# Optimization experiments

Measured on AMD Instinct MI355X. Metric: run time of the kernel, lower is better.

## Reference

```python
import jax, jax.numpy as jnp
import numpy as np

DIM = 1024
HEADS = 16
DH = DIM // HEADS
SEQ = 1024
MEM_LEN = 1024
CMEM_LEN = 256
RATIO = 4
SCALE = DH ** -0.5
LN_EPS = 1e-5


def shift(x):
    # x: [b,h,i,j] -> relative-position shift trick
    b, h, i, j = x.shape
    x = jnp.concatenate([x, jnp.zeros((b, h, i, i), x.dtype)], axis=-1)
    l = i + j - 1
    x = x.reshape(b, h, -1)
    pad = (-x.shape[-1]) % l
    x = jnp.concatenate([x, jnp.zeros((b, h, pad), x.dtype)], axis=-1)
    x = x.reshape(b, h, -1, l)
    return x[:, :, :i, i - 1:]


def layer_norm(x, g, b):
    mu = jnp.mean(x, axis=-1, keepdims=True)
    var = jnp.var(x, axis=-1, keepdims=True)
    return (x - mu) * jax.lax.rsqrt(var + LN_EPS) * g + b


def setup_inputs() -> dict:
    key = jax.random.key(0)
    ks = jax.random.split(key, 12)
    B = 4
    KV = CMEM_LEN + MEM_LEN + SEQ
    std = 0.02
    return {
        'x': jax.random.normal(ks[0], (B, SEQ, DIM), jnp.float32),
        'mem': jax.random.normal(ks[1], (B, MEM_LEN, DIM), jnp.float32),
        'cmem': jax.random.normal(ks[2], (B, CMEM_LEN, DIM), jnp.float32),
        'pos_embed': jax.random.normal(ks[3], (HEADS, KV, DH), jnp.float32),
        'input_mask': jnp.ones((B, SEQ), jnp.bool_),
        'Wq': jax.random.normal(ks[4], (DIM, DIM), jnp.float32) * std,
        'Wkv': jax.random.normal(ks[5], (DIM, 2 * DIM), jnp.float32) * std,
        'Wout': jax.random.normal(ks[6], (DIM, DIM), jnp.float32) * std,
        'bout': jnp.zeros((DIM,), jnp.float32),
        'ln_g': jnp.ones((DIM,), jnp.float32),
        'ln_b': jnp.zeros((DIM,), jnp.float32),
        'conv_w': jax.random.normal(ks[7], (DIM, DIM, RATIO), jnp.float32) * std,
        'conv_b': jnp.zeros((DIM,), jnp.float32),
    }


def reference(x, mem, cmem, pos_embed, input_mask, Wq, Wkv, Wout, bout, ln_g, ln_b, conv_w, conv_b):
    b, t, e = x.shape
    mem_len, cmem_len = mem.shape[1], cmem.shape[1]
    total_mem = mem_len + cmem_len

    q = x @ Wq  # [b,t,e]
    kv_input = jnp.concatenate([cmem, mem, x], axis=1)  # [b,kv,e]
    kv_len = kv_input.shape[1]
    kv = kv_input @ Wkv
    k, v = jnp.split(kv, 2, axis=-1)

    def merge_heads(u):
        return u.reshape(u.shape[0], u.shape[1], HEADS, DH).transpose(0, 2, 1, 3)

    q, k, v = merge_heads(q), merge_heads(k), merge_heads(v)  # [b,h,*,dh]

    dots = jnp.einsum('bhid,bhjd->bhij', q, k) * SCALE  # [b,h,t,kv]
    mask_value = -jnp.finfo(dots.dtype).max

    pe = pos_embed[:, -kv_len:].astype(q.dtype)
    pos_dots = jnp.einsum('bhid,hjd->bhij', q, pe) * SCALE
    dots = dots + shift(pos_dots)

    # input mask (memory columns always visible)
    imask = input_mask[:, None, :, None] & input_mask[:, None, None, :]  # [b,1,t,t]
    imask = jnp.concatenate([jnp.ones((b, 1, t, total_mem), jnp.bool_), imask], axis=-1)
    dots = jnp.where(imask, dots, mask_value)

    # causal mask with memory offset
    causal = jnp.triu(jnp.ones((t, t + total_mem), jnp.bool_), k=1 + total_mem)
    dots = jnp.where(causal[None, None], mask_value, dots)

    attn = jax.nn.softmax(dots, axis=-1)
    out = jnp.einsum('bhij,bhjd->bhid', attn, v)
    out = out.transpose(0, 2, 1, 3).reshape(b, t, -1)
    logits = out @ Wout + bout
    logits = layer_norm(x + logits, ln_g, ln_b)

    # memory update (calc_memory=True, eval mode: no aux reconstruction loss)
    all_mem = jnp.concatenate([mem, x], axis=1)
    old_mem, new_mem = all_mem[:, :-MEM_LEN], all_mem[:, -MEM_LEN:]
    # old_mem length (mem_len+t-MEM_LEN) is a multiple of RATIO here -> no pad needed
    om = old_mem.transpose(0, 2, 1)  # [b,e,L]
    comp = jax.lax.conv_general_dilated(
        om, conv_w, window_strides=(RATIO,), padding='VALID',
        dimension_numbers=('NCH', 'OIH', 'NCH')) + conv_b[None, :, None]
    compressed_mem = comp.transpose(0, 2, 1)  # [b,L/ratio,e]
    all_cmem = jnp.concatenate([cmem, compressed_mem], axis=1)
    new_cmem = all_cmem[:, -CMEM_LEN:]

    aux_loss = jnp.zeros((1,), q.dtype)
    return logits, new_mem, new_cmem, aux_loss
```

## Files before the change

### kernel.cpp

```cpp
#include <hip/hip_runtime.h>
#include <stdint.h>

typedef __attribute__((ext_vector_type(8))) short short8;
typedef __attribute__((ext_vector_type(4))) short short4_;
typedef __attribute__((ext_vector_type(4))) float floatx4;

#define MFMA16(a,b,c) __builtin_amdgcn_mfma_f32_16x16x32_bf16((a),(b),(c),0,0,0)

__device__ __forceinline__ short f2b(float f) {
  union { float f; uint32_t u; } v; v.f = f;
  uint32_t r = v.u + 0x7fffu + ((v.u >> 16) & 1u);
  return (short)(r >> 16);
}

__device__ __forceinline__ unsigned cvt_pk_bf16(float a, float b) {
  unsigned r;
  asm("v_cvt_pk_bf16_f32 %0, %1, %2" : "=v"(r) : "v"(a), "v"(b));
  return r;
}


__global__ __launch_bounds__(256) void pack_kvin(const float* __restrict__ x,
    const float* __restrict__ mem, const float* __restrict__ cmem,
    short* __restrict__ out) {
  long idx = (long)blockIdx.x * 256 + threadIdx.x;
  long base = idx * 4;
  if (base >= 9437184L) return;
  int b = (int)(base / 2359296L);
  int rem = (int)(base - (long)b * 2359296L);
  int r = rem >> 10, c = rem & 1023;
  const float* src;
  if (r < 256)       src = cmem + ((long)b * 256  + r)          * 1024 + c;
  else if (r < 1280) src = mem  + ((long)b * 1024 + (r - 256))  * 1024 + c;
  else               src = x    + ((long)b * 1024 + (r - 1280)) * 1024 + c;
  float4 v = *(const float4*)src;
  short4_ o; o.x = f2b(v.x); o.y = f2b(v.y); o.z = f2b(v.z); o.w = f2b(v.w);
  *(short4_*)(out + base) = o;
}

__global__ __launch_bounds__(256) void pack_cvt(const float* __restrict__ in,
    short* __restrict__ out, long n4) {
  long idx = (long)blockIdx.x * 256 + threadIdx.x;
  if (idx >= n4) return;
  long base = idx * 4;
  float4 v = *(const float4*)(in + base);
  short4_ o; o.x = f2b(v.x); o.y = f2b(v.y); o.z = f2b(v.z); o.w = f2b(v.w);
  *(short4_*)(out + base) = o;
}

__global__ __launch_bounds__(256) void pack_convw(const float* __restrict__ cw,
    short* __restrict__ out) {
  long idx = (long)blockIdx.x * 256 + threadIdx.x;
  long base = idx * 4;
  if (base >= 4194304L) return;
  int co = (int)(base >> 12);
  int r  = (int)(base & 4095);
  int tt = r >> 10, ci = r & 1023;
  const float* s = cw + (long)co * 4096 + tt;
  short4_ o;
  o.x = f2b(s[(ci + 0) * 4]); o.y = f2b(s[(ci + 1) * 4]);
  o.z = f2b(s[(ci + 2) * 4]); o.w = f2b(s[(ci + 3) * 4]);
  *(short4_*)(out + base) = o;
}

__global__ __launch_bounds__(256) void transpose_w(const float* __restrict__ in,
    short* __restrict__ out, int R, int C) {
  __shared__ float tile[32][33];
  int bx = blockIdx.x << 5, by = blockIdx.y << 5;
  int tx = threadIdx.x, ty = threadIdx.y;
#pragma unroll
  for (int yy = 0; yy < 4; ++yy)
    tile[ty + 8 * yy][tx] = in[(long)(by + ty + 8 * yy) * C + bx + tx];
  __syncthreads();
#pragma unroll
  for (int yy = 0; yy < 4; ++yy)
    out[(long)(bx + ty + 8 * yy) * R + by + tx] = f2b(tile[tx][ty + 8 * yy]);
}

__global__ __launch_bounds__(256) void transpose_v(const short* __restrict__ in,
    short* __restrict__ out) {
  __shared__ short tile[32][33];
  int bh = blockIdx.z;
  int j0 = blockIdx.x << 5, d0 = blockIdx.y << 5;
  int tx = threadIdx.x, ty = threadIdx.y;
  const short* ip = in + (long)bh * 147456;
  short* op = out + (long)bh * 147456;
#pragma unroll
  for (int yy = 0; yy < 4; ++yy)
    tile[ty + 8 * yy][tx] = ip[(long)(j0 + ty + 8 * yy) * 64 + d0 + tx];
  __syncthreads();
#pragma unroll
  for (int yy = 0; yy < 4; ++yy)
    op[(long)(d0 + ty + 8 * yy) * 2304 + j0 + tx] = tile[tx][ty + 8 * yy];
}

template<int MODE>
__global__ __launch_bounds__(256) void gemm_bt(
    const short* __restrict__ A, const short* __restrict__ Bt,
    float* __restrict__ Cf, short* __restrict__ Ck, short* __restrict__ Cv,
    const float* __restrict__ bias,
    int M, int N, int K, int a_rpb, long a_bstride, int a_row0, int a_lda) {
  __shared__ __align__(16) short As[128][40];
  __shared__ __align__(16) short Bs[128][40];
  int t = threadIdx.x;
  int w = t >> 6, lane = t & 63;
  int wr = (w >> 1) << 6, wc = (w & 1) << 6;
  int lrow = lane & 15, lk8 = (lane >> 4) << 3, lq4 = (lane >> 4) << 2;
  int rowblk = blockIdx.y << 7, colblk = blockIdx.x << 7;

  floatx4 acc[4][4];
#pragma unroll
  for (int i = 0; i < 4; ++i)
#pragma unroll
    for (int j = 0; j < 4; ++j) acc[i][j] = (floatx4){0.f, 0.f, 0.f, 0.f};

  int r0 = t >> 2, kc0 = (t & 3) << 3;
  int r1 = r0 + 64;
  int gr0 = rowblk + r0, gr1 = rowblk + r1;
  int b0 = gr0 / a_rpb, rr0 = gr0 - b0 * a_rpb;
  int b1 = gr1 / a_rpb, rr1 = gr1 - b1 * a_rpb;
  const short* a0p = A + b0 * a_bstride + (long)(a_row0 + rr0) * a_lda + kc0;
  const short* a1p = A + b1 * a_bstride + (long)(a_row0 + rr1) * a_lda + kc0;
  const short* b0p = Bt + (long)(colblk + r0) * K + kc0;
  const short* b1p = Bt + (long)(colblk + r1) * K + kc0;

  for (int k0 = 0; k0 < K; k0 += 32) {
    __syncthreads();
    *(uint4*)(&As[r0][kc0]) = *(const uint4*)(a0p + k0);
    *(uint4*)(&As[r1][kc0]) = *(const uint4*)(a1p + k0);
    *(uint4*)(&Bs[r0][kc0]) = *(const uint4*)(b0p + k0);
    *(uint4*)(&Bs[r1][kc0]) = *(const uint4*)(b1p + k0);
    __syncthreads();
    short8 af[4], bf[4];
#pragma unroll
    for (int mm = 0; mm < 4; ++mm) af[mm] = *(const short8*)(&As[wr + (mm << 4) + lrow][lk8]);
#pragma unroll
    for (int nn = 0; nn < 4; ++nn) bf[nn] = *(const short8*)(&Bs[wc + (nn << 4) + lrow][lk8]);
#pragma unroll
    for (int mm = 0; mm < 4; ++mm)
#pragma unroll
      for (int nn = 0; nn < 4; ++nn)
        acc[mm][nn] = MFMA16(af[mm], bf[nn], acc[mm][nn]);
  }

#pragma unroll
  for (int mm = 0; mm < 4; ++mm) {
#pragma unroll
    for (int nn = 0; nn < 4; ++nn) {
#pragma unroll
      for (int q = 0; q < 4; ++q) {
        int grow = rowblk + wr + (mm << 4) + lq4 + q;
        int gcol = colblk + wc + (nn << 4) + (lane & 15);
        float v = acc[mm][nn][q];
        if (MODE == 0) {
          Cf[(long)grow * N + gcol] = v + bias[gcol];
        } else if (MODE == 1) {
          int b = grow >> 10, i = grow & 1023, hh = gcol >> 6, d = gcol & 63;
          Ck[(((long)(b * 16 + hh)) * 1024 + i) * 64 + d] = f2b(v * 0.125f);
        } else {
          int b = grow / 2304, j = grow - b * 2304;
          if (gcol < 1024) {
            int hh = gcol >> 6, d = gcol & 63;
            Ck[(((long)(b * 16 + hh)) * 2304 + j) * 64 + d] = f2b(v);
          } else {
            int c2 = gcol - 1024, hh = c2 >> 6, d = c2 & 63;
            Cv[(((long)(b * 16 + hh)) * 2304 + j) * 64 + d] = f2b(v);
          }
        }
      }
    }
  }
}

__global__ __launch_bounds__(256) void gemm64_bias(const short* __restrict__ A,
    const short* __restrict__ Bt, float* __restrict__ Cf,
    const float* __restrict__ bias,
    int N, int K, int a_rpb, long a_bstride, int a_lda) {
  __shared__ __align__(16) short As[64][40];
  __shared__ __align__(16) short Bs[64][40];
  int t = threadIdx.x;
  int w = t >> 6, lane = t & 63;
  int wr = (w >> 1) << 5, wc = (w & 1) << 5;
  int lrow = lane & 15, lk8 = (lane >> 4) << 3, lq4 = (lane >> 4) << 2;
  int rowblk = blockIdx.y << 6, colblk = blockIdx.x << 6;
  floatx4 acc[2][2];
#pragma unroll
  for (int i = 0; i < 2; ++i)
#pragma unroll
    for (int j = 0; j < 2; ++j) acc[i][j] = (floatx4){0.f, 0.f, 0.f, 0.f};

  int r0 = t >> 2, kc0 = (t & 3) << 3;
  int gr0 = rowblk + r0;
  int b0 = gr0 / a_rpb, rr0 = gr0 - b0 * a_rpb;
  const short* a0p = A + b0 * a_bstride + (long)rr0 * a_lda + kc0;
  const short* b0p = Bt + (long)(colblk + r0) * K + kc0;

  for (int k0 = 0; k0 < K; k0 += 32) {
    __syncthreads();
    *(uint4*)(&As[r0][kc0]) = *(const uint4*)(a0p + k0);
    *(uint4*)(&Bs[r0][kc0]) = *(const uint4*)(b0p + k0);
    __syncthreads();
    short8 af[2], bf[2];
#pragma unroll
    for (int mm = 0; mm < 2; ++mm) af[mm] = *(const short8*)(&As[wr + (mm << 4) + lrow][lk8]);
#pragma unroll
    for (int nn = 0; nn < 2; ++nn) bf[nn] = *(const short8*)(&Bs[wc + (nn << 4) + lrow][lk8]);
#pragma unroll
    for (int mm = 0; mm < 2; ++mm)
#pragma unroll
      for (int nn = 0; nn < 2; ++nn)
        acc[mm][nn] = MFMA16(af[mm], bf[nn], acc[mm][nn]);
  }
#pragma unroll
  for (int mm = 0; mm < 2; ++mm)
#pragma unroll
    for (int nn = 0; nn < 2; ++nn)
#pragma unroll
      for (int q = 0; q < 4; ++q) {
        int grow = rowblk + wr + (mm << 4) + lq4 + q;
        int gcol = colblk + wc + (nn << 4) + (lane & 15);
        Cf[(long)grow * N + gcol] = acc[mm][nn][q] + bias[gcol];
      }
}

__global__ __launch_bounds__(64, 2) void attn_kernel(
    const short* __restrict__ q_r, const short* __restrict__ k_r,
    const short* __restrict__ vt, const short* __restrict__ pe_b,
    short* __restrict__ attn_out) {
  __shared__ float T_skew[2][16][97];
  __shared__ __align__(16) short P_lds[2][16][72];
  int blk = blockIdx.x;
  int ib = blk & 31, bh = blk >> 5;
  int b = bh >> 4, h = bh & 15;
  int i0 = ib << 5;
  int lane = threadIdx.x;
  int l = lane & 15, g = lane >> 4;
  int k8 = g << 3;

  const short* qb = q_r + ((long)(bh * 1024 + i0) << 6);
  short8 qf[2][2];
#pragma unroll
  for (int m = 0; m < 2; ++m) {
    qf[m][0] = *(const short8*)(qb + (((m << 4) + l) << 6) + k8);
    qf[m][1] = *(const short8*)(qb + (((m << 4) + l) << 6) + 32 + k8);
  }

  const short* kb = k_r + (long)bh * 147456;
  const short* vb = vt  + (long)bh * 147456;
  const short* pb = pe_b + (long)h * 147456;

  floatx4 o[2][4];
#pragma unroll
  for (int m = 0; m < 2; ++m)
#pragma unroll
    for (int dc = 0; dc < 4; ++dc) o[m][dc] = (floatx4){0.f, 0.f, 0.f, 0.f};
  float mreg[2] = {-1e30f, -1e30f};
  float lreg[2] = {0.f, 0.f};

  int ntiles = ((i0 + 1311) >> 6) + 1;
  for (int tt = 0; tt < ntiles; ++tt) {
    int j0 = tt << 6;
    short8 kf[4][2];
#pragma unroll
    for (int jt = 0; jt < 4; ++jt) {
      const short* kr = kb + ((long)(j0 + (jt << 4) + l) << 6);
      kf[jt][0] = *(const short8*)(kr + k8);
      kf[jt][1] = *(const short8*)(kr + 32 + k8);
    }
    short8 vf[4][2];
#pragma unroll
    for (int dc = 0; dc < 4; ++dc) {
      const short* vr = vb + (long)((dc << 4) + l) * 2304 + j0;
      vf[dc][0] = *(const short8*)(vr + k8);
      vf[dc][1] = *(const short8*)(vr + 32 + k8);
    }
#pragma unroll
    for (int m = 0; m < 2; ++m) {
      int i0c = i0 + (m << 4);
      if (j0 > i0c + 1295) continue;
      floatx4 s[4];
#pragma unroll
      for (int jt = 0; jt < 4; ++jt) {
        s[jt] = (floatx4){0.f, 0.f, 0.f, 0.f};
        s[jt] = MFMA16(kf[jt][0], qf[m][0], s[jt]);
        s[jt] = MFMA16(kf[jt][1], qf[m][1], s[jt]);
      }
      int rb = j0 - i0c + 1008;
#pragma unroll
      for (int pt = 0; pt < 5; ++pt) {
        int r = rb + (pt << 4) + l;
        r = r < 2303 ? r : 2303;
        const short* pr = pb + ((long)r << 6);
        floatx4 ta = {0.f, 0.f, 0.f, 0.f};
        ta = MFMA16(qf[m][0], *(const short8*)(pr + k8), ta);
        ta = MFMA16(qf[m][1], *(const short8*)(pr + 32 + k8), ta);
        int row0 = g << 2;
#pragma unroll
        for (int q = 0; q < 4; ++q)
          T_skew[m][row0 + q][(pt << 4) + l + row0 + q] = ta[q];
      }
      __syncthreads();
      int lim = i0c + l + 1280 - j0;
      float p[4][4];
      float mx = -1e30f;
#pragma unroll
      for (int jt = 0; jt < 4; ++jt)
#pragma unroll
        for (int q = 0; q < 4; ++q) {
          int jl = (jt << 4) + (g << 2) + q;
          float v = s[jt][q] + T_skew[m][l][jl + 15];
          v = (jl > lim) ? -1e30f : v;
          p[jt][q] = v;
          mx = fmaxf(mx, v);
        }
      mx = fmaxf(mx, __shfl_xor(mx, 16));
      mx = fmaxf(mx, __shfl_xor(mx, 32));
      if (__any(mx - mreg[m] > 8.f)) {
        float nm = fmaxf(mreg[m], mx);
        float al = __expf(mreg[m] - nm);
#pragma unroll
        for (int dc = 0; dc < 4; ++dc) o[m][dc] *= al;
        lreg[m] *= al;
        mreg[m] = nm;
      }
      float rs = 0.f;
#pragma unroll
      for (int jt = 0; jt < 4; ++jt)
#pragma unroll
        for (int q = 0; q < 4; ++q) {
          p[jt][q] = __expf(p[jt][q] - mreg[m]);
          rs += p[jt][q];
        }
      rs += __shfl_xor(rs, 16);
      rs += __shfl_xor(rs, 32);
      lreg[m] += rs;
#pragma unroll
      for (int jt = 0; jt < 4; ++jt) {
        unsigned u0 = cvt_pk_bf16(p[jt][0], p[jt][1]);
        unsigned u1 = cvt_pk_bf16(p[jt][2], p[jt][3]);
        int c0 = (jt << 4) + (g << 2);
        *(unsigned*)&P_lds[m][l][c0]     = u0;
        *(unsigned*)&P_lds[m][l][c0 + 2] = u1;
      }
      __syncthreads();
      short8 pa0 = *(const short8*)&P_lds[m][l][k8];
      short8 pa1 = *(const short8*)&P_lds[m][l][32 + k8];
#pragma unroll
      for (int dc = 0; dc < 4; ++dc) {
        o[m][dc] = MFMA16(vf[dc][0], pa0, o[m][dc]);
        o[m][dc] = MFMA16(vf[dc][1], pa1, o[m][dc]);
      }
    }
  }
#pragma unroll
  for (int m = 0; m < 2; ++m) {
    float invl = 1.f / lreg[m];
    long rowbase = ((long)(b * 1024 + i0 + (m << 4) + l) << 10) + (h << 6) + (g << 2);
#pragma unroll
    for (int dc = 0; dc < 4; ++dc) {
      uint2 u;
      u.x = cvt_pk_bf16(o[m][dc][0] * invl, o[m][dc][1] * invl);
      u.y = cvt_pk_bf16(o[m][dc][2] * invl, o[m][dc][3] * invl);
      *(uint2*)(attn_out + rowbase + (dc << 4)) = u;
    }
  }
}

__global__ __launch_bounds__(256) void ln_kernel(const float* __restrict__ x,
    const float* __restrict__ lp, const float* __restrict__ g,
    const float* __restrict__ bb, float* __restrict__ out) {
  int row = blockIdx.x, t = threadIdx.x;
  long base = (long)row * 1024 + t * 4;
  float4 a = *(const float4*)(x + base);
  float4 bo = *(const float4*)(lp + base);
  float v0 = a.x + bo.x, v1 = a.y + bo.y, v2 = a.z + bo.z, v3 = a.w + bo.w;
  float s1 = v0 + v1 + v2 + v3;
  float s2 = v0 * v0 + v1 * v1 + v2 * v2 + v3 * v3;
#pragma unroll
  for (int off = 1; off < 64; off <<= 1) {
    s1 += __shfl_xor(s1, off);
    s2 += __shfl_xor(s2, off);
  }
  __shared__ float r1[4], r2[4];
  int w = t >> 6;
  if ((t & 63) == 0) { r1[w] = s1; r2[w] = s2; }
  __syncthreads();
  float S1 = r1[0] + r1[1] + r1[2] + r1[3];
  float S2 = r2[0] + r2[1] + r2[2] + r2[3];
  float mu = S1 * (1.f / 1024.f);
  float var = S2 * (1.f / 1024.f) - mu * mu;
  float rs = rsqrtf(var + 1e-5f);
  float4 gv = *(const float4*)(g + t * 4);
  float4 bv = *(const float4*)(bb + t * 4);
  float4 o;
  o.x = (v0 - mu) * rs * gv.x + bv.x;
  o.y = (v1 - mu) * rs * gv.y + bv.y;
  o.z = (v2 - mu) * rs * gv.z + bv.z;
  o.w = (v3 - mu) * rs * gv.w + bv.w;
  *(float4*)(out + base) = o;
}

__global__ __launch_bounds__(256) void copy_x(const float* __restrict__ x,
    float* __restrict__ outmem, float* __restrict__ aux) {
  long i = (long)blockIdx.x * 256 + threadIdx.x;
  ((float4*)outmem)[i] = ((const float4*)x)[i];
  if (i == 0) aux[0] = 0.f;
}

extern "C" void kernel_launch(void* const* d_in, const int* in_sizes, int n_in,
                              void* d_out, int out_size, void* d_ws, size_t ws_size,
                              hipStream_t stream) {
  const float* x    = (const float*)d_in[0];
  const float* mem  = (const float*)d_in[1];
  const float* cmem = (const float*)d_in[2];
  const float* pe   = (const float*)d_in[3];
  const float* Wq   = (const float*)d_in[5];
  const float* Wkv  = (const float*)d_in[6];
  const float* Wout = (const float*)d_in[7];
  const float* bout = (const float*)d_in[8];
  const float* lng  = (const float*)d_in[9];
  const float* lnb  = (const float*)d_in[10];
  const float* cw   = (const float*)d_in[11];
  const float* cb   = (const float*)d_in[12];

  char* ws = (char*)d_ws;
  short* kvin_b = (short*)(ws + 0);
  short* q_r    = (short*)(ws + 18874368);
  short* k_r    = (short*)(ws + 27262976);
  short* vtp    = (short*)(ws + 46137344);
  short* v_r    = (short*)(ws + 65011712);
  short* pe_b   = (short*)(ws + 83886080);
  short* wq_t   = (short*)(ws + 88604672);
  short* wkv_t  = (short*)(ws + 90701824);
  short* wout_t = (short*)(ws + 94896128);
  short* cw_t   = (short*)(ws + 96993280);
  short* attn_o = (short*)(ws + 105381888);
  float* lpre   = (float*)(ws + 113770496);

  float* out_logits = (float*)d_out;
  float* out_mem    = out_logits + 4194304;
  float* out_cmem   = out_logits + 8388608;
  float* out_aux    = out_logits + 9437184;

  pack_kvin<<<9216, 256, 0, stream>>>(x, mem, cmem, kvin_b);
  pack_cvt<<<2304, 256, 0, stream>>>(pe, pe_b, 589824);
  transpose_w<<<dim3(32, 32), dim3(32, 8), 0, stream>>>(Wq, wq_t, 1024, 1024);
  transpose_w<<<dim3(64, 32), dim3(32, 8), 0, stream>>>(Wkv, wkv_t, 1024, 2048);
  transpose_w<<<dim3(32, 32), dim3(32, 8), 0, stream>>>(Wout, wout_t, 1024, 1024);
  pack_convw<<<4096, 256, 0, stream>>>(cw, cw_t);

  gemm_bt<1><<<dim3(8, 32), 256, 0, stream>>>(kvin_b, wq_t, nullptr, q_r, nullptr,
      nullptr, 4096, 1024, 1024, 1024, 2359296L, 1280, 1024);
  gemm_bt<2><<<dim3(16, 72), 256, 0, stream>>>(kvin_b, wkv_t, nullptr, k_r, v_r,
      nullptr, 9216, 2048, 1024, 2304, 2359296L, 0, 1024);
  transpose_v<<<dim3(72, 2, 64), dim3(32, 8), 0, stream>>>(v_r, vtp);

  attn_kernel<<<2048, 64, 0, stream>>>(q_r, k_r, vtp, pe_b, attn_o);

  gemm_bt<0><<<dim3(8, 32), 256, 0, stream>>>(attn_o, wout_t, lpre, nullptr, nullptr,
      bout, 4096, 1024, 1024, 4096, 0L, 0, 1024);
  ln_kernel<<<4096, 256, 0, stream>>>(x, lpre, lng, lnb, out_logits);

  copy_x<<<4096, 256, 0, stream>>>(x, out_mem, out_aux);

  gemm64_bias<<<dim3(16, 16), 256, 0, stream>>>(kvin_b + 262144, cw_t, out_cmem,
      cb, 1024, 4096, 256, 2359296L, 4096);
}
```

Baseline: 641.2 us.

## Use direct global-to-LDS loads in GEMMs and restructure attention kernel

Both GEMM kernels now stage A/B tiles through global_load_lds (direct global-to-shared copies) instead of register round trips, and drop the LDS row padding that such copies require. The attention kernel shares one T_skew/P_lds buffer across both 16-row chunks and removes the __syncthreads between chunk phases, since a block is a single wavefront. It also double-buffers K fragments in registers across tiles and remaps block indices so neighbouring blocks spread across heads and batches. Risks: unpadded LDS rows may cause bank conflicts on MFMA fragment reads, and the larger register footprint from double buffering plus the relaxed launch bounds can reduce occupancy.

```diff
diff --git a/kernel.cpp b/kernel.cpp
--- a/kernel.cpp
+++ b/kernel.cpp
@@ -17,6 +17,10 @@
   unsigned r;
   asm("v_cvt_pk_bf16_f32 %0, %1, %2" : "=v"(r) : "v"(a), "v"(b));
   return r;
+}
+
+__device__ __forceinline__ void gload_lds16(const short* g, short* l) {
+  __builtin_amdgcn_global_load_lds((const unsigned int*)g, (unsigned int*)l, 16, 0, 0);
 }
 
 
@@ -100,8 +104,8 @@
     float* __restrict__ Cf, short* __restrict__ Ck, short* __restrict__ Cv,
     const float* __restrict__ bias,
     int M, int N, int K, int a_rpb, long a_bstride, int a_row0, int a_lda) {
-  __shared__ __align__(16) short As[128][40];
-  __shared__ __align__(16) short Bs[128][40];
+  __shared__ __align__(16) short As[128][32];
+  __shared__ __align__(16) short Bs[128][32];
   int t = threadIdx.x;
   int w = t >> 6, lane = t & 63;
   int wr = (w >> 1) << 6, wc = (w & 1) << 6;
@@ -114,22 +118,25 @@
 #pragma unroll
     for (int j = 0; j < 4; ++j) acc[i][j] = (floatx4){0.f, 0.f, 0.f, 0.f};
 
-  int r0 = t >> 2, kc0 = (t & 3) << 3;
-  int r1 = r0 + 64;
-  int gr0 = rowblk + r0, gr1 = rowblk + r1;
-  int b0 = gr0 / a_rpb, rr0 = gr0 - b0 * a_rpb;
-  int b1 = gr1 / a_rpb, rr1 = gr1 - b1 * a_rpb;
-  const short* a0p = A + b0 * a_bstride + (long)(a_row0 + rr0) * a_lda + kc0;
-  const short* a1p = A + b1 * a_bstride + (long)(a_row0 + rr1) * a_lda + kc0;
-  const short* b0p = Bt + (long)(colblk + r0) * K + kc0;
-  const short* b1p = Bt + (long)(colblk + r1) * K + kc0;
+  int srow = (w << 5) + (lane >> 2), kcol = (lane & 3) << 3;
+  int gA0 = rowblk + srow, gA1 = gA0 + 16;
+  int bA0 = gA0 / a_rpb, rA0 = gA0 - bA0 * a_rpb;
+  int bA1 = gA1 / a_rpb, rA1 = gA1 - bA1 * a_rpb;
+  const short* a0p = A + bA0 * a_bstride + (long)(a_row0 + rA0) * a_lda + kcol;
+  const short* a1p = A + bA1 * a_bstride + (long)(a_row0 + rA1) * a_lda + kcol;
+  const short* b0p = Bt + (long)(colblk + srow) * K + kcol;
+  const short* b1p = b0p + (long)16 * K;
+  short* lA0 = &As[(w << 5)][0];
+  short* lA1 = &As[(w << 5) + 16][0];
+  short* lB0 = &Bs[(w << 5)][0];
+  short* lB1 = &Bs[(w << 5) + 16][0];
 
   for (int k0 = 0; k0 < K; k0 += 32) {
     __syncthreads();
-    *(uint4*)(&As[r0][kc0]) = *(const uint4*)(a0p + k0);
-    *(uint4*)(&As[r1][kc0]) = *(const uint4*)(a1p + k0);
-    *(uint4*)(&Bs[r0][kc0]) = *(const uint4*)(b0p + k0);
-    *(uint4*)(&Bs[r1][kc0]) = *(const uint4*)(b1p + k0);
+    gload_lds16(a0p + k0, lA0);
+    gload_lds16(a1p + k0, lA1);
+    gload_lds16(b0p + k0, lB0);
+    gload_lds16(b1p + k0, lB1);
     __syncthreads();
     short8 af[4], bf[4];
 #pragma unroll
@@ -176,8 +183,8 @@
     const short* __restrict__ Bt, float* __restrict__ Cf,
     const float* __restrict__ bias,
     int N, int K, int a_rpb, long a_bstride, int a_lda) {
-  __shared__ __align__(16) short As[64][40];
-  __shared__ __align__(16) short Bs[64][40];
+  __shared__ __align__(16) short As[64][32];
+  __shared__ __align__(16) short Bs[64][32];
   int t = threadIdx.x;
   int w = t >> 6, lane = t & 63;
   int wr = (w >> 1) << 5, wc = (w & 1) << 5;
@@ -189,16 +196,18 @@
 #pragma unroll
     for (int j = 0; j < 2; ++j) acc[i][j] = (floatx4){0.f, 0.f, 0.f, 0.f};
 
-  int r0 = t >> 2, kc0 = (t & 3) << 3;
-  int gr0 = rowblk + r0;
-  int b0 = gr0 / a_rpb, rr0 = gr0 - b0 * a_rpb;
-  const short* a0p = A + b0 * a_bstride + (long)rr0 * a_lda + kc0;
-  const short* b0p = Bt + (long)(colblk + r0) * K + kc0;
+  int srow = (w << 4) + (lane >> 2), kcol = (lane & 3) << 3;
+  int gA0 = rowblk + srow;
+  int bA0 = gA0 / a_rpb, rA0 = gA0 - bA0 * a_rpb;
+  const short* a0p = A + bA0 * a_bstride + (long)rA0 * a_lda + kcol;
+  const short* b0p = Bt + (long)(colblk + srow) * K + kcol;
+  short* lA0 = &As[(w << 4)][0];
+  short* lB0 = &Bs[(w << 4)][0];
 
   for (int k0 = 0; k0 < K; k0 += 32) {
     __syncthreads();
-    *(uint4*)(&As[r0][kc0]) = *(const uint4*)(a0p + k0);
-    *(uint4*)(&Bs[r0][kc0]) = *(const uint4*)(b0p + k0);
+    gload_lds16(a0p + k0, lA0);
+    gload_lds16(b0p + k0, lB0);
     __syncthreads();
     short8 af[2], bf[2];
 #pragma unroll
@@ -223,13 +232,14 @@
       }
 }
 
-__global__ __launch_bounds__(64, 2) void attn_kernel(
+__global__ __launch_bounds__(64) void attn_kernel(
     const short* __restrict__ q_r, const short* __restrict__ k_r,
     const short* __restrict__ vt, const short* __restrict__ pe_b,
     short* __restrict__ attn_out) {
-  __shared__ float T_skew[2][16][97];
-  __shared__ __align__(16) short P_lds[2][16][72];
-  int blk = blockIdx.x;
+  __shared__ float T_skew[16][97];
+  __shared__ __align__(16) short P_lds[16][72];
+  int p = blockIdx.x;
+  int blk = ((p & 7) << 8) | (p >> 3);
   int ib = blk & 31, bh = blk >> 5;
   int b = bh >> 4, h = bh & 15;
   int i0 = ib << 5;
@@ -249,24 +259,101 @@
   const short* vb = vt  + (long)bh * 147456;
   const short* pb = pe_b + (long)h * 147456;
 
-  floatx4 o[2][4];
-#pragma unroll
-  for (int m = 0; m < 2; ++m)
-#pragma unroll
-    for (int dc = 0; dc < 4; ++dc) o[m][dc] = (floatx4){0.f, 0.f, 0.f, 0.f};
-  float mreg[2] = {-1e30f, -1e30f};
-  float lreg[2] = {0.f, 0.f};
+  floatx4 o0[4], o1[4];
+#pragma unroll
+  for (int dc = 0; dc < 4; ++dc) {
+    o0[dc] = (floatx4){0.f, 0.f, 0.f, 0.f};
+    o1[dc] = (floatx4){0.f, 0.f, 0.f, 0.f};
+  }
+  float m0r = -1e30f, m1r = -1e30f, l0r = 0.f, l1r = 0.f;
 
   int ntiles = ((i0 + 1311) >> 6) + 1;
-  for (int tt = 0; tt < ntiles; ++tt) {
+
+  short8 kfA[4][2], kfB[4][2];
+#pragma unroll
+  for (int jt = 0; jt < 4; ++jt) {
+    const short* kr = kb + ((long)((jt << 4) + l) << 6);
+    kfA[jt][0] = *(const short8*)(kr + k8);
+    kfA[jt][1] = *(const short8*)(kr + 32 + k8);
+  }
+
+  auto chunk = [&](int i0c, short8 (&kf)[4][2], short8 (&vf)[4][2],
+                   short8 (&qfm)[2], float& mreg, float& lreg,
+                   floatx4 (&oo)[4], int j0) {
+    floatx4 s[4];
+#pragma unroll
+    for (int jt = 0; jt < 4; ++jt) {
+      s[jt] = (floatx4){0.f, 0.f, 0.f, 0.f};
+      s[jt] = MFMA16(kf[jt][0], qfm[0], s[jt]);
+      s[jt] = MFMA16(kf[jt][1], qfm[1], s[jt]);
+    }
+    int rb = j0 - i0c + 1008;
+#pragma unroll
+    for (int pt = 0; pt < 5; ++pt) {
+      int r = rb + (pt << 4) + l;
+      r = r < 2303 ? r : 2303;
+      const short* pr = pb + ((long)r << 6);
+      floatx4 ta = {0.f, 0.f, 0.f, 0.f};
+      ta = MFMA16(qfm[0], *(const short8*)(pr + k8), ta);
+      ta = MFMA16(qfm[1], *(const short8*)(pr + 32 + k8), ta);
+      int row0 = g << 2;
+#pragma unroll
+      for (int q = 0; q < 4; ++q)
+        T_skew[row0 + q][(pt << 4) + l + row0 + q] = ta[q];
+    }
+    int lim = i0c + l + 1280 - j0;
+    float pv[4][4];
+    float mx = -1e30f;
+#pragma unroll
+    for (int jt = 0; jt < 4; ++jt)
+#pragma unroll
+      for (int q = 0; q < 4; ++q) {
+        int jl = (jt << 4) + (g << 2) + q;
+        float v = s[jt][q] + T_skew[l][jl + 15];
+        v = (jl > lim) ? -1e30f : v;
+        pv[jt][q] = v;
+        mx = fmaxf(mx, v);
+      }
+    mx = fmaxf(mx, __shfl_xor(mx, 16));
+    mx = fmaxf(mx, __shfl_xor(mx, 32));
+    if (__any(mx - mreg > 8.f)) {
+      float nm = fmaxf(mreg, mx);
+      float al = __expf(mreg - nm);
+#pragma unroll
+      for (int dc = 0; dc < 4; ++dc) oo[dc] *= al;
+      lreg *= al;
+      mreg = nm;
+    }
+    float rs = 0.f;
+#pragma unroll
+    for (int jt = 0; jt < 4; ++jt)
+#pragma unroll
+      for (int q = 0; q < 4; ++q) {
+        pv[jt][q] = __expf(pv[jt][q] - mreg);
+        rs += pv[jt][q];
+      }
+    rs += __shfl_xor(rs, 16);
+    rs += __shfl_xor(rs, 32);
+    lreg += rs;
+#pragma unroll
+    for (int jt = 0; jt < 4; ++jt) {
+      unsigned u0 = cvt_pk_bf16(pv[jt][0], pv[jt][1]);
+      unsigned u1 = cvt_pk_bf16(pv[jt][2], pv[jt][3]);
+      int c0 = (jt << 4) + (g << 2);
+      *(unsigned*)&P_lds[l][c0]     = u0;
+      *(unsigned*)&P_lds[l][c0 + 2] = u1;
+    }
+    short8 pa0 = *(const short8*)&P_lds[l][k8];
+    short8 pa1 = *(const short8*)&P_lds[l][32 + k8];
+#pragma unroll
+    for (int dc = 0; dc < 4; ++dc) {
+      oo[dc] = MFMA16(vf[dc][0], pa0, oo[dc]);
+      oo[dc] = MFMA16(vf[dc][1], pa1, oo[dc]);
+    }
+  };
+
+  auto body = [&](short8 (&kfC)[4][2], short8 (&kfN)[4][2], int tt) {
     int j0 = tt << 6;
-    short8 kf[4][2];
-#pragma unroll
-    for (int jt = 0; jt < 4; ++jt) {
-      const short* kr = kb + ((long)(j0 + (jt << 4) + l) << 6);
-      kf[jt][0] = *(const short8*)(kr + k8);
-      kf[jt][1] = *(const short8*)(kr + 32 + k8);
-    }
     short8 vf[4][2];
 #pragma unroll
     for (int dc = 0; dc < 4; ++dc) {
@@ -274,93 +361,38 @@
       vf[dc][0] = *(const short8*)(vr + k8);
       vf[dc][1] = *(const short8*)(vr + 32 + k8);
     }
-#pragma unroll
-    for (int m = 0; m < 2; ++m) {
-      int i0c = i0 + (m << 4);
-      if (j0 > i0c + 1295) continue;
-      floatx4 s[4];
+    if (tt + 1 < ntiles) {
+      int j0n = j0 + 64;
 #pragma unroll
       for (int jt = 0; jt < 4; ++jt) {
-        s[jt] = (floatx4){0.f, 0.f, 0.f, 0.f};
-        s[jt] = MFMA16(kf[jt][0], qf[m][0], s[jt]);
-        s[jt] = MFMA16(kf[jt][1], qf[m][1], s[jt]);
+        const short* kr = kb + ((long)(j0n + (jt << 4) + l) << 6);
+        kfN[jt][0] = *(const short8*)(kr + k8);
+        kfN[jt][1] = *(const short8*)(kr + 32 + k8);
       }
-      int rb = j0 - i0c + 1008;
-#pragma unroll
-      for (int pt = 0; pt < 5; ++pt) {
-        int r = rb + (pt << 4) + l;
-        r = r < 2303 ? r : 2303;
-        const short* pr = pb + ((long)r << 6);
-        floatx4 ta = {0.f, 0.f, 0.f, 0.f};
-        ta = MFMA16(qf[m][0], *(const short8*)(pr + k8), ta);
-        ta = MFMA16(qf[m][1], *(const short8*)(pr + 32 + k8), ta);
-        int row0 = g << 2;
-#pragma unroll
-        for (int q = 0; q < 4; ++q)
-          T_skew[m][row0 + q][(pt << 4) + l + row0 + q] = ta[q];
-      }
-      __syncthreads();
-      int lim = i0c + l + 1280 - j0;
-      float p[4][4];
-      float mx = -1e30f;
-#pragma unroll
-      for (int jt = 0; jt < 4; ++jt)
-#pragma unroll
-        for (int q = 0; q < 4; ++q) {
-          int jl = (jt << 4) + (g << 2) + q;
-          float v = s[jt][q] + T_skew[m][l][jl + 15];
-          v = (jl > lim) ? -1e30f : v;
-          p[jt][q] = v;
-          mx = fmaxf(mx, v);
-        }
-      mx = fmaxf(mx, __shfl_xor(mx, 16));
-      mx = fmaxf(mx, __shfl_xor(mx, 32));
-      if (__any(mx - mreg[m] > 8.f)) {
-        float nm = fmaxf(mreg[m], mx);
-        float al = __expf(mreg[m] - nm);
-#pragma unroll
-        for (int dc = 0; dc < 4; ++dc) o[m][dc] *= al;
-        lreg[m] *= al;
-        mreg[m] = nm;
-      }
-      float rs = 0.f;
-#pragma unroll
-      for (int jt = 0; jt < 4; ++jt)
-#pragma unroll
-        for (int q = 0; q < 4; ++q) {
-          p[jt][q] = __expf(p[jt][q] - mreg[m]);
-          rs += p[jt][q];
-        }
-      rs += __shfl_xor(rs, 16);
-      rs += __shfl_xor(rs, 32);
-      lreg[m] += rs;
-#pragma unroll
-      for (int jt = 0; jt < 4; ++jt) {
-        unsigned u0 = cvt_pk_bf16(p[jt][0], p[jt][1]);
-        unsigned u1 = cvt_pk_bf16(p[jt][2], p[jt][3]);
-        int c0 = (jt << 4) + (g << 2);
-        *(unsigned*)&P_lds[m][l][c0]     = u0;
-        *(unsigned*)&P_lds[m][l][c0 + 2] = u1;
-      }
-      __syncthreads();
-      short8 pa0 = *(const short8*)&P_lds[m][l][k8];
-      short8 pa1 = *(const short8*)&P_lds[m][l][32 + k8];
-#pragma unroll
-      for (int dc = 0; dc < 4; ++dc) {
-        o[m][dc] = MFMA16(vf[dc][0], pa0, o[m][dc]);
-        o[m][dc] = MFMA16(vf[dc][1], pa1, o[m][dc]);
-      }
-    }
-  }
+    }
+    if (j0 <= i0 + 1295)
+      chunk(i0, kfC, vf, qf[0], m0r, l0r, o0, j0);
+    chunk(i0 + 16, kfC, vf, qf[1], m1r, l1r, o1, j0);
+  };
+
+  int tt = 0;
+  while (true) {
+    body(kfA, kfB, tt);
+    if (++tt >= ntiles) break;
+    body(kfB, kfA, tt);
+    if (++tt >= ntiles) break;
+  }
+
 #pragma unroll
   for (int m = 0; m < 2; ++m) {
-    float invl = 1.f / lreg[m];
+    float invl = 1.f / (m == 0 ? l0r : l1r);
+    floatx4* oo = (m == 0) ? o0 : o1;
     long rowbase = ((long)(b * 1024 + i0 + (m << 4) + l) << 10) + (h << 6) + (g << 2);
 #pragma unroll
     for (int dc = 0; dc < 4; ++dc) {
       uint2 u;
-      u.x = cvt_pk_bf16(o[m][dc][0] * invl, o[m][dc][1] * invl);
-      u.y = cvt_pk_bf16(o[m][dc][2] * invl, o[m][dc][3] * invl);
+      u.x = cvt_pk_bf16(oo[dc][0] * invl, oo[dc][1] * invl);
+      u.y = cvt_pk_bf16(oo[dc][2] * invl, oo[dc][3] * invl);
       *(uint2*)(attn_out + rowbase + (dc << 4)) = u;
     }
   }
```

Measured after the change: 657.8 us. 1.03x slower.
